# Kernel tuning notes

Hardware: AMD Instinct MI355X
Metric: run time of the kernel (lower is better)

Reference implementation:

```python
import jax, jax.numpy as jnp
import numpy as np

N = 100000      # nodes
IN_DIM = 128    # input feature dim
HID = 64        # hidden_dim / out_dim per head
HEADS = 4
E_RAND = 1600000  # random edges; self-loops appended -> E = E_RAND + N
SCALES = 3


def setup_inputs() -> dict:
    key = jax.random.key(0)
    ks = jax.random.split(key, 12)
    h = jax.random.normal(ks[0], (N, IN_DIM), dtype=jnp.float32)
    src = jax.random.randint(ks[1], (E_RAND,), 0, N)
    dst = jax.random.randint(ks[2], (E_RAND,), 0, N)
    loop = jnp.arange(N)
    src = jnp.concatenate([src, loop])  # self-loops ensure every dst has a mailbox
    dst = jnp.concatenate([dst, loop])
    frac_cover_mat = jax.random.randint(ks[3], (N, SCALES), 0, N)
    # learned params (bias=False everywhere); xavier-ish scaling
    layer1_fc = jax.random.normal(ks[4], (HEADS, HID, IN_DIM), jnp.float32) / np.sqrt(IN_DIM)
    layer1_attn = jax.random.normal(ks[5], (HEADS, 2 * HID), jnp.float32) * 0.1
    layer2_fc = jax.random.normal(ks[6], (HID, HID * HEADS), jnp.float32) / np.sqrt(HID * HEADS)
    layer2_attn = jax.random.normal(ks[7], (2 * HID,), jnp.float32) * 0.1
    frac_w = jax.random.normal(ks[8], (SCALES, HID, IN_DIM), jnp.float32) / np.sqrt(IN_DIM)
    frac_final_w = jax.random.normal(ks[9], (HID, SCALES * HID), jnp.float32) / np.sqrt(SCALES * HID)
    fc2_w = jax.random.normal(ks[10], (HID, 2 * HID), jnp.float32) / np.sqrt(2 * HID)
    return {"h": h, "src": src, "dst": dst, "frac_cover_mat": frac_cover_mat,
            "layer1_fc": layer1_fc, "layer1_attn": layer1_attn,
            "layer2_fc": layer2_fc, "layer2_attn": layer2_attn,
            "frac_w": frac_w, "frac_final_w": frac_final_w, "fc2_w": fc2_w}


def _gat_layer(z, src, dst, attn_w, n):
    # attn(cat([z_src, z_dst])) == z_src @ a_src + z_dst @ a_dst  (bias-free Linear)
    d = z.shape[1]
    e = jax.nn.leaky_relu(z[src] @ attn_w[:d] + z[dst] @ attn_w[d:])  # [E]
    # segment softmax over incoming edges of each dst node
    m = jax.ops.segment_max(e, dst, num_segments=n)
    ex = jnp.exp(e - m[dst])
    denom = jax.ops.segment_sum(ex, dst, num_segments=n)
    alpha = ex / denom[dst]                                   # [E]
    return jax.ops.segment_sum(alpha[:, None] * z[src], dst, num_segments=n)  # [N, d]


def reference(h, src, dst, frac_cover_mat,
              layer1_fc, layer1_attn, layer2_fc, layer2_attn,
              frac_w, frac_final_w, fc2_w):
    n = h.shape[0]
    # layer1: multi-head GAT, merge='cat'
    heads = []
    for i in range(layer1_fc.shape[0]):
        z = h @ layer1_fc[i].T                                # [N, HID]
        heads.append(_gat_layer(z, src, dst, layer1_attn[i], n))
    h_nei = jax.nn.elu(jnp.concatenate(heads, axis=1))        # [N, HID*HEADS]
    # layer2: single-head GAT
    z2 = h_nei @ layer2_fc.T                                  # [N, HID]
    h_nei = _gat_layer(z2, src, dst, layer2_attn, n)          # [N, HID]
    # fractal layer (dropout = identity in eval)
    h_all = [h[frac_cover_mat[:, s]] @ frac_w[s].T for s in range(frac_w.shape[0])]
    h_frac = jnp.concatenate(h_all, axis=1) @ frac_final_w.T  # [N, HID]
    # fc2 on cat([h_nei, h_frac]); dropout identity
    h_global = jnp.concatenate([h_nei, h_frac], axis=1) @ fc2_w.T  # [N, HID]
    # AvgPooling over single graph -> [1, HID]
    return jnp.mean(h_global, axis=0, keepdims=True)
```

## Files before the change

kernel.cpp:

```cpp
#include <hip/hip_runtime.h>
#include <math.h>


#define CAP 128

typedef unsigned int  uint_t;
typedef unsigned short ushort_t;
typedef __attribute__((ext_vector_type(8))) short short8;
typedef __attribute__((ext_vector_type(4))) float floatx4;
typedef __attribute__((ext_vector_type(2))) float floatx2;

__device__ __forceinline__ unsigned xcc_id(){
  unsigned x;
  asm volatile("s_getreg_b32 %0, hwreg(HW_REG_XCC_ID)" : "=s"(x));
  return x & 7u;
}
__device__ __forceinline__ float wred_sum(float v){
#pragma unroll
  for (int o = 1; o < 64; o <<= 1) v += __shfl_xor(v, o, 64);
  return v;
}
__device__ __forceinline__ float lrelu(float x){ return x >= 0.f ? x : 0.01f*x; }
__device__ __forceinline__ ushort_t f2b(float f){
  uint_t u = __float_as_uint(f);
  u = (u + 0x7FFFu + ((u >> 16) & 1u)) >> 16;
  return (ushort_t)u;
}
__device__ __forceinline__ float b2f_lo(uint_t w){ return __uint_as_float(w << 16); }
__device__ __forceinline__ float b2f_hi(uint_t w){ return __uint_as_float(w & 0xFFFF0000u); }

__device__ __forceinline__ void agg8(uint2 u, float4 al,
    floatx2& c00, floatx2& c01, floatx2& c10, floatx2& c11){
  floatx2 p0 = __builtin_amdgcn_cvt_pk_f32_fp8(u.x, false);
  floatx2 p1 = __builtin_amdgcn_cvt_pk_f32_fp8(u.x, true);
  floatx2 p2 = __builtin_amdgcn_cvt_pk_f32_fp8(u.y, false);
  floatx2 p3 = __builtin_amdgcn_cvt_pk_f32_fp8(u.y, true);
  floatx2 aXY = {al.x, al.y}, aZW = {al.z, al.w};
  c00 += aXY * p0;
  c01 += aZW * p1;
  c10 += aXY * p2;
  c11 += aZW * p3;
}

__global__ void k_prep(const float* __restrict__ W1, const float* __restrict__ W2,
                       const float* __restrict__ a1, const float* __restrict__ a2,
                       const int* __restrict__ dstI, int E,
                       const int* __restrict__ fcm, int N3, int* __restrict__ cnt,
                       ushort_t* __restrict__ w1bp, float* __restrict__ v2,
                       int* __restrict__ deg8, int* __restrict__ rk, int PAD){
  __shared__ float v[8][128];
  const int bx = blockIdx.x, t = threadIdx.x;
  if (bx < 128){
    int idx = bx*256 + t;
    int j = idx & 7, lane = (idx >> 3) & 63, ks = (idx >> 9) & 3, tt = idx >> 11;
    int n = tt*16 + (lane & 15), k = ks*32 + (lane >> 4)*8 + j;
    int hh = tt >> 2, m = tt & 3;
    int pt = (m < 2) ? (hh*2 + m) : (8 + hh*2 + (m - 2));
    w1bp[((pt*4 + ks)*64 + lane)*8 + j] = f2b(W1[n*128 + k]);
  } else if (bx == 128){
    for (int o = t; o < 1024; o += 256){
      int col = o >> 7, k = o & 127, hh = col & 3, off = (col >> 2)*64;
      float s = 0.f;
      for (int n = 0; n < 64; n++) s += a1[hh*128 + off + n] * W1[(hh*64 + n)*128 + k];
      v[col][k] = s;
    }
    __syncthreads();
    for (int idx = t; idx < 2048; idx += 256){
      int j = idx & 7, lane = (idx >> 3) & 63, ks = idx >> 9;
      int col = lane & 15, k = ks*32 + (lane >> 4)*8 + j;
      w1bp[32768 + idx] = (col < 8) ? f2b(v[col][k]) : (ushort_t)0;
    }
  } else if (bx == 129){
    float s0 = 0.f, s1 = 0.f;
    for (int j = 0; j < 64; j++){
      float wjk = W2[j*256 + t];
      s0 += wjk * a2[j];
      s1 += wjk * a2[64 + j];
    }
    v2[t] = s0; v2[256 + t] = s1;
  } else {
    const int nb = gridDim.x - 130;
    const unsigned xcd = xcc_id();
    int* myDeg = deg8 + (size_t)xcd * PAD;
    for (int i = (bx-130)*256 + t; i < E; i += nb*256){
      int d = dstI[i];
      int r = __hip_atomic_fetch_add(&myDeg[d], 1, __ATOMIC_RELAXED,
                                     __HIP_MEMORY_SCOPE_WORKGROUP);
      rk[i] = (int)((xcd << 28) | (unsigned)r);
    }
    for (int i = (bx-130)*256 + t; i < N3; i += nb*256){
      int v3 = fcm[i];
      atomicAdd(&cnt[v3*3 + (i % 3)], 1);
    }
  }
}

__global__ __launch_bounds__(256) void k_scan1(const int* __restrict__ deg8,
    int* __restrict__ part, int PAD){
  __shared__ int tmp[256];
  int t = threadIdx.x, i = blockIdx.x*256 + t;
  int v = 0;
#pragma unroll
  for (int x = 0; x < 8; x++) v += deg8[(size_t)x*PAD + i];
  tmp[t] = v;
  __syncthreads();
  for (int off = 128; off > 0; off >>= 1){
    if (t < off) tmp[t] += tmp[t+off];
    __syncthreads();
  }
  if (t == 0) part[blockIdx.x] = tmp[0];
}
__global__ __launch_bounds__(512) void k_scan2(int* __restrict__ part, int B){
  __shared__ int tmp[512];
  int t = threadIdx.x;
  int v = (t < B) ? part[t] : 0;
  tmp[t] = v; __syncthreads();
  for (int off = 1; off < 512; off <<= 1){
    int x = (t >= off) ? tmp[t-off] : 0;
    __syncthreads();
    tmp[t] += x;
    __syncthreads();
  }
  if (t < B) part[t] = tmp[t] - v;
}
__global__ __launch_bounds__(256) void k_scan3(const int* __restrict__ deg8,
    const int* __restrict__ part, int* __restrict__ rowptr,
    int* __restrict__ base8, int PAD){
  __shared__ int tmp[256];
  int t = threadIdx.x, i = blockIdx.x*256 + t;
  int d8[8]; int v = 0;
#pragma unroll
  for (int x = 0; x < 8; x++){ d8[x] = deg8[(size_t)x*PAD + i]; v += d8[x]; }
  tmp[t] = v; __syncthreads();
  for (int off = 1; off < 256; off <<= 1){
    int x = (t >= off) ? tmp[t-off] : 0;
    __syncthreads();
    tmp[t] += x;
    __syncthreads();
  }
  int excl = tmp[t] - v + part[blockIdx.x];
  rowptr[i] = excl;
  int run = excl;
#pragma unroll
  for (int x = 0; x < 8; x++){ base8[(size_t)x*PAD + i] = run; run += d8[x]; }
}

__global__ __launch_bounds__(512, 4) void k_mega(const float* __restrict__ h,
    const ushort_t* __restrict__ w1bp,
    uint_t* __restrict__ z8, float* __restrict__ s1s, float* __restrict__ s1d, int N,
    const int* __restrict__ srcI, const int* __restrict__ dstI,
    const int* __restrict__ rk, const int* __restrict__ base8, int PAD,
    int* __restrict__ csr, int E,
    int Gg, int Gs, int G, int step,
    const int* __restrict__ cnt, float* __restrict__ accFrac)
{
  static __shared__ __align__(16) char smem[36864];
  const int tid = threadIdx.x;
  const int id = (int)(((unsigned long long)blockIdx.x * (unsigned)step) % (unsigned)G);
  if (id < Gg){
    ushort_t* ldsB = (ushort_t*)smem;
    const int wave = tid >> 6, lane = tid & 63;
    const int quad = lane >> 4, l16 = lane & 15;
    const int row0 = id*128 + wave*16;
    const bool act = row0 < N;
    const int ar = act ? ((row0 + l16 < N) ? (row0 + l16) : (N - 1)) : 0;
    short8 AHI[4], ALO[4];
    if (act){
#pragma unroll
      for (int ks = 0; ks < 4; ks++){
        const float* ap = &h[(size_t)ar*128 + ks*32 + quad*8];
        float4 v0 = *(const float4*)ap;
        float4 v1 = *(const float4*)(ap + 4);
        float vv[8] = {v0.x,v0.y,v0.z,v0.w,v1.x,v1.y,v1.z,v1.w};
#pragma unroll
        for (int j = 0; j < 8; j++){
          ushort_t hb = f2b(vv[j]);
          float hf = __uint_as_float((uint_t)hb << 16);
          AHI[ks][j] = (short)hb;
          ALO[ks][j] = (short)f2b(vv[j] - hf);
        }
      }
    }
#pragma unroll
    for (int half = 0; half < 2; half++){
      __syncthreads();
      {
        const int cnt4 = half ? 2304 : 2048;
        const uint4* src = (const uint4*)w1bp + (half ? 2048 : 0);
        uint4* dst = (uint4*)ldsB;
        for (int i = tid; i < cnt4; i += 512) dst[i] = src[i];
      }
      __syncthreads();
      if (!act) continue;
      const int nt = half ? 9 : 8;
      floatx4 c[9];
#pragma unroll
      for (int i = 0; i < 9; i++) c[i] = (floatx4){0.f,0.f,0.f,0.f};
#pragma unroll
      for (int ks = 0; ks < 4; ks++){
        for (int i = 0; i < nt; i++){
          short8 b = *(const short8*)&ldsB[(size_t)((i*4 + ks)*64 + lane)*8];
          c[i] = __builtin_amdgcn_mfma_f32_16x16x32_bf16(AHI[ks], b, c[i], 0, 0, 0);
        }
        if (half){
          short8 b = *(const short8*)&ldsB[(size_t)((8*4 + ks)*64 + lane)*8];
          c[8] = __builtin_amdgcn_mfma_f32_16x16x32_bf16(ALO[ks], b, c[8], 0, 0, 0);
        }
      }
      const int m0 = half ? 2 : 0;
#pragma unroll
      for (int i = 0; i < 4; i++){
        const int r = row0 + quad*4 + i;
        if (r >= N) continue;
#pragma unroll
        for (int dm = 0; dm < 2; dm++){
          int u = 0;
          u = __builtin_amdgcn_cvt_pk_fp8_f32(c[0*2+dm][i], c[1*2+dm][i], u, false);
          u = __builtin_amdgcn_cvt_pk_fp8_f32(c[2*2+dm][i], c[3*2+dm][i], u, true);
          z8[(size_t)r*64 + (m0+dm)*16 + l16] = (uint_t)u;
        }
        if (half){
          const float sv = c[8][i];
          if (l16 < 4) s1s[r*4 + l16] = sv;
          else if (l16 < 8) s1d[r*4 + (l16 - 4)] = sv;
        }
      }
    }
  } else if (id < Gg + Gs){
    const int i = (id - Gg)*512 + tid;
    if (i < E){
      const int d = dstI[i];
      const uint_t u = (uint_t)rk[i];
      const int p = base8[(size_t)(u >> 28)*PAD + d] + (int)(u & 0x0FFFFFFFu);
      csr[p] = srcI[i];
    }
  } else {
    float (*red)[384] = (float(*)[384])smem;
    const int wave = tid >> 6, lane = tid & 63;
    const int g = lane >> 5, li = lane & 31;
    const int Gf = G - Gg - Gs;
    const int stream0 = (id - Gg - Gs)*16 + wave*2 + g;
    const int step16 = Gf * 16;
    float4 a0 = {0,0,0,0}, a1 = {0,0,0,0}, a2 = {0,0,0,0};
    for (int n = stream0; n < N; n += step16){
      const float w0 = (float)cnt[n*3];
      const float w1 = (float)cnt[n*3+1];
      const float w2 = (float)cnt[n*3+2];
      float4 v = *(const float4*)&h[(size_t)n*128 + li*4];
      a0.x += w0*v.x; a0.y += w0*v.y; a0.z += w0*v.z; a0.w += w0*v.w;
      a1.x += w1*v.x; a1.y += w1*v.y; a1.z += w1*v.z; a1.w += w1*v.w;
      a2.x += w2*v.x; a2.y += w2*v.y; a2.z += w2*v.z; a2.w += w2*v.w;
    }
    const int w16 = wave*2 + g;
    *(float4*)&red[w16][0*128 + li*4] = a0;
    *(float4*)&red[w16][1*128 + li*4] = a1;
    *(float4*)&red[w16][2*128 + li*4] = a2;
    __syncthreads();
    for (int i = tid; i < 384; i += 512){
      float v = 0.f;
#pragma unroll
      for (int w = 0; w < 16; w++) v += red[w][i];
      atomicAdd(&accFrac[i], v);
    }
  }
}

__global__ __launch_bounds__(256) void k_gat1(
    const uint_t* __restrict__ z8, const float* __restrict__ s1src, const float* __restrict__ s1dst,
    const int* __restrict__ rowptr, const int* __restrict__ csr, const float* __restrict__ v2,
    uint_t* __restrict__ hneib, float* __restrict__ s2s, float* __restrict__ s2d, int N, int dbase)
{
  __shared__ int   sbuf[4][CAP];
  __shared__ __align__(16) float4 ebuf[4][CAP];
  __shared__ float v2s[512];
  const int tid = threadIdx.x;
  v2s[tid] = v2[tid];
  v2s[tid + 256] = v2[tid + 256];
  __syncthreads();
  const int wave = tid >> 6, lane = tid & 63;
  const int dst = (dbase + blockIdx.x)*4 + wave;
  if (dst >= N) return;
  const int beg = rowptr[dst];
  const int deg = rowptr[dst+1] - beg;
  const float4 sd = *(const float4*)&s1dst[dst*4];
  float t0=0.f,t1=0.f,t2=0.f,t3=0.f;
  for (int j = lane; j < deg; j += 64){
    int s = csr[beg+j];
    float4 sv = *(const float4*)&s1src[s*4];
    float4 a;
    a.x = __expf(lrelu(sv.x+sd.x)); a.y = __expf(lrelu(sv.y+sd.y));
    a.z = __expf(lrelu(sv.z+sd.z)); a.w = __expf(lrelu(sv.w+sd.w));
    if (j < CAP){ sbuf[wave][j] = s*64; ebuf[wave][j] = a; }
    t0 += a.x; t1 += a.y; t2 += a.z; t3 += a.w;
  }
  const float inv[4] = {1.f/wred_sum(t0), 1.f/wred_sum(t1), 1.f/wred_sum(t2), 1.f/wred_sum(t3)};
  const int eh = lane >> 5, li = lane & 31;
  floatx2 c00 = {0.f,0.f}, c01 = {0.f,0.f}, c10 = {0.f,0.f}, c11 = {0.f,0.f};
  if (deg <= CAP){
    const int j0 = (eh < deg) ? eh : 0;
    int offc = sbuf[wave][j0];
    float4 alc = ebuf[wave][j0];
    uint2 uc = *((const uint2*)(z8 + offc) + li);
    for (int jj = 0; jj + 2 <= deg; jj += 2){
      const int jn = jj + 2 + eh;
      const int jnc = (jn < deg) ? jn : (jj + eh);
      const int offn = sbuf[wave][jnc];
      const float4 aln = ebuf[wave][jnc];
      const uint2 un = *((const uint2*)(z8 + offn) + li);
      agg8(uc, alc, c00, c01, c10, c11);
      uc = un; alc = aln;
    }
    if ((deg & 1) && eh == 0)
      agg8(uc, alc, c00, c01, c10, c11);
  } else {
    for (int jj = 0; jj < deg; jj += 2){
      const int j = jj + eh;
      const bool v = j < deg;
      const int jc = v ? j : jj;
      int off; float4 al;
      if (jc < CAP){ off = sbuf[wave][jc]; al = ebuf[wave][jc]; }
      else {
        int s = csr[beg+jc];
        off = s*64;
        float4 sv = *(const float4*)&s1src[s*4];
        al.x = __expf(lrelu(sv.x+sd.x)); al.y = __expf(lrelu(sv.y+sd.y));
        al.z = __expf(lrelu(sv.z+sd.z)); al.w = __expf(lrelu(sv.w+sd.w));
      }
      if (!v){ al.x=0.f; al.y=0.f; al.z=0.f; al.w=0.f; }
      uint2 u = *((const uint2*)(z8 + off) + li);
      agg8(u, al, c00, c01, c10, c11);
    }
  }
  float acc[2][4] = {{c00.x, c00.y, c01.x, c01.y},
                     {c10.x, c10.y, c11.x, c11.y}};
#pragma unroll
  for (int k = 0; k < 2; k++)
#pragma unroll
    for (int hh = 0; hh < 4; hh++) acc[k][hh] += __shfl_xor(acc[k][hh], 32, 64);
  const float* vv = &v2s[eh*256];
  float p = 0.f;
#pragma unroll
  for (int hh = 0; hh < 4; hh++){
    float e0 = acc[0][hh]*inv[hh]; e0 = e0 > 0.f ? e0 : expm1f(e0);
    float e1 = acc[1][hh]*inv[hh]; e1 = e1 > 0.f ? e1 : expm1f(e1);
    p += e0 * vv[hh*64 + 2*li] + e1 * vv[hh*64 + 2*li + 1];
    if ((hh >> 1) == eh)
      hneib[(size_t)dst*128 + hh*32 + li] = (uint_t)f2b(e0) | ((uint_t)f2b(e1) << 16);
  }
#pragma unroll
  for (int o = 1; o < 32; o <<= 1) p += __shfl_xor(p, o, 64);
  if (lane == 0)  s2s[dst] = p;
  if (lane == 32) s2d[dst] = p;
}

__global__ __launch_bounds__(256) void k_aw2(
    const float* __restrict__ s2s, const float* __restrict__ s2d,
    const int* __restrict__ rowptr, const int* __restrict__ csr,
    float* __restrict__ wsrc8, int N)
{
  __shared__ int   sbuf[4][CAP];
  __shared__ float ebuf[4][CAP];
  const unsigned xcd = xcc_id();
  float* ws = wsrc8 + (size_t)xcd * N;
  const int wave = threadIdx.x >> 6, lane = threadIdx.x & 63;
  const int dst = blockIdx.x*4 + wave;
  if (dst >= N) return;
  const int beg = rowptr[dst], deg = rowptr[dst+1] - beg;
  const float sd = s2d[dst];
  float ts = 0.f;
  for (int j = lane; j < deg; j += 64){
    int s = csr[beg+j];
    float a = __expf(lrelu(s2s[s] + sd));
    if (j < CAP){ sbuf[wave][j] = s; ebuf[wave][j] = a; }
    ts += a;
  }
  const float inv = 1.f/wred_sum(ts);
  for (int j = lane; j < deg; j += 64){
    int s; float a;
    if (j < CAP){ s = sbuf[wave][j]; a = ebuf[wave][j]; }
    else { s = csr[beg+j]; a = __expf(lrelu(s2s[s] + sd)); }
    __hip_atomic_fetch_add(&ws[s], a * inv, __ATOMIC_RELAXED,
                           __HIP_MEMORY_SCOPE_WORKGROUP);
  }
}

__global__ __launch_bounds__(256) void k_hsum(const uint_t* __restrict__ hneib,
    const float* __restrict__ wsrc8, float* __restrict__ acc256, int N)
{
  __shared__ float pr[512];
  const int t = threadIdx.x;
  const int h2 = t >> 7, p = t & 127;
  float a0 = 0.f, a1 = 0.f;
  const int step = gridDim.x * 2;
  for (int n = blockIdx.x*2 + h2; n < N; n += step){
    float wn = 0.f;
#pragma unroll
    for (int x = 0; x < 8; x++) wn += wsrc8[(size_t)x*N + n];
    uint_t u = hneib[(size_t)n*128 + p];
    a0 += wn * b2f_lo(u);
    a1 += wn * b2f_hi(u);
  }
  pr[h2*256 + 2*p]     = a0;
  pr[h2*256 + 2*p + 1] = a1;
  __syncthreads();
  float v = pr[t] + pr[256 + t];
  int pp = t >> 1;
  int d = (pp >> 5)*64 + 2*(pp & 31) + (t & 1);
  atomicAdd(&acc256[d], v);
}

__global__ __launch_bounds__(256) void k_finalize(const float* __restrict__ acc256,
    const float* __restrict__ accFrac, const float* __restrict__ W2,
    const float* __restrict__ frw, const float* __restrict__ frf,
    const float* __restrict__ fc2, float* __restrict__ out, float invN)
{
  __shared__ float mh[256], nei[64], g[384], mm[192], hfrac[64];
  int t = threadIdx.x;
  mh[t] = acc256[t] * invN;
  for (int i = t; i < 384; i += 256) g[i] = accFrac[i] * invN;
  __syncthreads();
  if (t < 64){
    float s = 0.f;
    for (int k = 0; k < 256; k++) s += W2[t*256 + k] * mh[k];
    nei[t] = s;
  }
  for (int i = t; i < 192; i += 256){
    int s = i >> 6, d = i & 63;
    const float* w = frw + (size_t)(s*64 + d)*128;
    const float* gs = g + s*128;
    float sum = 0.f;
    for (int k = 0; k < 128; k++) sum += gs[k]*w[k];
    mm[i] = sum;
  }
  __syncthreads();
  if (t < 64){
    float s = 0.f;
    for (int k = 0; k < 192; k++) s += mm[k]*frf[t*192 + k];
    hfrac[t] = s;
  }
  __syncthreads();
  if (t < 64){
    float o = 0.f;
    for (int k = 0; k < 64; k++)
      o += fc2[t*128 + k]*nei[k] + fc2[t*128 + 64 + k]*hfrac[k];
    out[t] = o;
  }
}

extern "C" void kernel_launch(void* const* d_in, const int* in_sizes, int n_in,
                              void* d_out, int out_size, void* d_ws, size_t ws_size,
                              hipStream_t stream)
{
  const float* h    = (const float*)d_in[0];
  const int*   srcI = (const int*)  d_in[1];
  const int*   dstI = (const int*)  d_in[2];
  const int*   fcm  = (const int*)  d_in[3];
  const float* l1fc = (const float*)d_in[4];
  const float* l1at = (const float*)d_in[5];
  const float* l2fc = (const float*)d_in[6];
  const float* l2at = (const float*)d_in[7];
  const float* frw  = (const float*)d_in[8];
  const float* frf  = (const float*)d_in[9];
  const float* fc2  = (const float*)d_in[10];
  float* out = (float*)d_out;
  (void)n_in; (void)out_size; (void)ws_size;

  const int N = in_sizes[0] / 128;
  const int E = in_sizes[1];
  const int B = (N + 256) / 256;
  const int PAD = B * 256;

  char* w = (char*)d_ws;
  size_t off = 0;
  auto alloc = [&](size_t bytes) -> char* {
    char* p = w + off; off = (off + bytes + 255) & ~(size_t)255; return p;
  };
  uint_t* z8    = (uint_t*)alloc((size_t)N*64*4);
  uint_t* hneib = (uint_t*)alloc((size_t)N*128*4);
  int*    rk    = (int*)hneib;
  float* s1s  = (float*)alloc((size_t)N*4*4);
  float* s1d  = (float*)alloc((size_t)N*4*4);
  float* s2s  = (float*)alloc((size_t)N*4);
  float* s2d  = (float*)alloc((size_t)N*4);
  int*   deg8    = (int*)  alloc((size_t)8*PAD*4);
  int*   cnt     = (int*)  alloc((size_t)N*3*4);
  float* wsrc8   = (float*)alloc((size_t)8*N*4);
  float* acc256  = (float*)alloc(256*4);
  float* accFrac = (float*)alloc(384*4);
  const size_t zbytes = (size_t)((char*)accFrac + 384*4 - (char*)deg8);
  int*   rowptr = (int*)alloc((size_t)PAD*4);
  int*   base8  = (int*)alloc((size_t)8*PAD*4);
  int*   part   = (int*)alloc(512*4);
  int*   csr    = (int*)alloc((size_t)E*4);
  ushort_t* w1bp = (ushort_t*)alloc(34816*2);
  float* v2     = (float*)alloc(512*4);

  hipMemsetAsync(deg8, 0, zbytes, stream);

  hipLaunchKernelGGL(k_prep,  dim3(130 + 512), dim3(256), 0, stream,
                     l1fc, l2fc, l1at, l2at, dstI, E, fcm, 3*N, cnt, w1bp, v2,
                     deg8, rk, PAD);
  hipLaunchKernelGGL(k_scan1, dim3(B),   dim3(256), 0, stream, deg8, part, PAD);
  hipLaunchKernelGGL(k_scan2, dim3(1),   dim3(512), 0, stream, part, B);
  hipLaunchKernelGGL(k_scan3, dim3(B),   dim3(256), 0, stream, deg8, part,
                     rowptr, base8, PAD);

  const int Gg = (N + 127) / 128;
  const int Gs = (E + 511) / 512;
  const int Gf = 512;
  const int G  = Gg + Gs + Gf;
  int step = (int)(G * 0.618) | 1;
  auto gcd = [](int a, int b){ while (b){ int t = a % b; a = b; b = t; } return a; };
  while (gcd(step, G) != 1) step += 2;

  hipLaunchKernelGGL(k_mega,  dim3(G), dim3(512), 0, stream,
                     h, w1bp, z8, s1s, s1d, N,
                     srcI, dstI, rk, base8, PAD, csr, E, Gg, Gs, G, step,
                     cnt, accFrac);
  const int nb  = (N + 3) / 4;
  const int nb3 = nb / 3;
  hipLaunchKernelGGL(k_gat1,  dim3(nb3),        dim3(256), 0, stream,
                     z8, s1s, s1d, rowptr, csr, v2, hneib, s2s, s2d, N, 0);
  hipLaunchKernelGGL(k_gat1,  dim3(nb3),        dim3(256), 0, stream,
                     z8, s1s, s1d, rowptr, csr, v2, hneib, s2s, s2d, N, nb3);
  hipLaunchKernelGGL(k_gat1,  dim3(nb - 2*nb3), dim3(256), 0, stream,
                     z8, s1s, s1d, rowptr, csr, v2, hneib, s2s, s2d, N, 2*nb3);
  hipLaunchKernelGGL(k_aw2,   dim3(nb),         dim3(256), 0, stream,
                     s2s, s2d, rowptr, csr, wsrc8, N);
  hipLaunchKernelGGL(k_hsum,  dim3(608),        dim3(256), 0, stream,
                     hneib, wsrc8, acc256, N);
  hipLaunchKernelGGL(k_finalize, dim3(1),       dim3(256), 0, stream,
                     acc256, accFrac, l2fc, frw, frf, fc2, out, 1.0f/(float)N);
}
```

Baseline: 527.4 us.

## Replace layer-2 float scatter atomics with a source-sorted CSC gather sum

Layer-2 per-source weights used to be accumulated with float atomics into per-XCD copies of a weight array. They are now built from a second, source-keyed CSC: k_mega gains a block group that counts source degrees and ranks, and scan kernels build source row pointers. k_aw2 writes each normalized alpha into its CSC slot, and a new k_wsum kernel sums each source's slots. This removes contended float atomics and the 8-way partial reduction, at the cost of extra index arrays, more memory traffic, three more scan launches and one more kernel. The k_gat1 split also changes from three launches to two.

```diff
diff --git a/kernel.cpp b/kernel.cpp
--- a/kernel.cpp
+++ b/kernel.cpp
@@ -95,13 +95,13 @@
   }
 }
 
-__global__ __launch_bounds__(256) void k_scan1(const int* __restrict__ deg8,
+__global__ __launch_bounds__(256) void k_scan1(const int* __restrict__ dp,
     int* __restrict__ part, int PAD){
   __shared__ int tmp[256];
   int t = threadIdx.x, i = blockIdx.x*256 + t;
   int v = 0;
 #pragma unroll
-  for (int x = 0; x < 8; x++) v += deg8[(size_t)x*PAD + i];
+  for (int x = 0; x < 8; x++) v += dp[(size_t)x*PAD + i];
   tmp[t] = v;
   __syncthreads();
   for (int off = 128; off > 0; off >>= 1){
@@ -123,14 +123,14 @@
   }
   if (t < B) part[t] = tmp[t] - v;
 }
-__global__ __launch_bounds__(256) void k_scan3(const int* __restrict__ deg8,
-    const int* __restrict__ part, int* __restrict__ rowptr,
-    int* __restrict__ base8, int PAD){
+__global__ __launch_bounds__(256) void k_scan3(const int* __restrict__ dp,
+    const int* __restrict__ part, int* __restrict__ rowp,
+    int* __restrict__ basep, int PAD){
   __shared__ int tmp[256];
   int t = threadIdx.x, i = blockIdx.x*256 + t;
   int d8[8]; int v = 0;
 #pragma unroll
-  for (int x = 0; x < 8; x++){ d8[x] = deg8[(size_t)x*PAD + i]; v += d8[x]; }
+  for (int x = 0; x < 8; x++){ d8[x] = dp[(size_t)x*PAD + i]; v += d8[x]; }
   tmp[t] = v; __syncthreads();
   for (int off = 1; off < 256; off <<= 1){
     int x = (t >= off) ? tmp[t-off] : 0;
@@ -139,10 +139,10 @@
     __syncthreads();
   }
   int excl = tmp[t] - v + part[blockIdx.x];
-  rowptr[i] = excl;
+  rowp[i] = excl;
   int run = excl;
 #pragma unroll
-  for (int x = 0; x < 8; x++){ base8[(size_t)x*PAD + i] = run; run += d8[x]; }
+  for (int x = 0; x < 8; x++){ basep[(size_t)x*PAD + i] = run; run += d8[x]; }
 }
 
 __global__ __launch_bounds__(512, 4) void k_mega(const float* __restrict__ h,
@@ -150,8 +150,9 @@
     uint_t* __restrict__ z8, float* __restrict__ s1s, float* __restrict__ s1d, int N,
     const int* __restrict__ srcI, const int* __restrict__ dstI,
     const int* __restrict__ rk, const int* __restrict__ base8, int PAD,
-    int* __restrict__ csr, int E,
-    int Gg, int Gs, int G, int step,
+    int* __restrict__ csr, int* __restrict__ csrEid,
+    int* __restrict__ degS8, int* __restrict__ rkS, int E,
+    int Gg, int Gs, int Gh, int G, int step,
     const int* __restrict__ cnt, float* __restrict__ accFrac)
 {
   static __shared__ __align__(16) char smem[36864];
@@ -231,15 +232,25 @@
     if (i < E){
       const int d = dstI[i];
       const uint_t u = (uint_t)rk[i];
-      const int p = base8[(size_t)(u >> 28)*PAD + d] + (int)(u & 0x0FFFFFFFu);
-      csr[p] = srcI[i];
+      const int pD = base8[(size_t)(u >> 28)*PAD + d] + (int)(u & 0x0FFFFFFFu);
+      csr[pD]    = srcI[i];
+      csrEid[pD] = i;
+    }
+  } else if (id < Gg + Gs + Gh){
+    const int i = (id - Gg - Gs)*512 + tid;
+    if (i < E){
+      const unsigned xcd = xcc_id();
+      int s = srcI[i];
+      int rs = __hip_atomic_fetch_add(&degS8[(size_t)xcd*PAD + s], 1,
+                                      __ATOMIC_RELAXED, __HIP_MEMORY_SCOPE_WORKGROUP);
+      rkS[i] = (int)((xcd << 28) | (unsigned)rs);
     }
   } else {
     float (*red)[384] = (float(*)[384])smem;
     const int wave = tid >> 6, lane = tid & 63;
     const int g = lane >> 5, li = lane & 31;
-    const int Gf = G - Gg - Gs;
-    const int stream0 = (id - Gg - Gs)*16 + wave*2 + g;
+    const int Gf = G - Gg - Gs - Gh;
+    const int stream0 = (id - Gg - Gs - Gh)*16 + wave*2 + g;
     const int step16 = Gf * 16;
     float4 a0 = {0,0,0,0}, a1 = {0,0,0,0}, a2 = {0,0,0,0};
     for (int n = stream0; n < N; n += step16){
@@ -356,12 +367,12 @@
 __global__ __launch_bounds__(256) void k_aw2(
     const float* __restrict__ s2s, const float* __restrict__ s2d,
     const int* __restrict__ rowptr, const int* __restrict__ csr,
-    float* __restrict__ wsrc8, int N)
+    const int* __restrict__ csrEid, const int* __restrict__ rkS,
+    const int* __restrict__ baseS8, int PAD,
+    float* __restrict__ alphaCSC, int N)
 {
   __shared__ int   sbuf[4][CAP];
   __shared__ float ebuf[4][CAP];
-  const unsigned xcd = xcc_id();
-  float* ws = wsrc8 + (size_t)xcd * N;
   const int wave = threadIdx.x >> 6, lane = threadIdx.x & 63;
   const int dst = blockIdx.x*4 + wave;
   if (dst >= N) return;
@@ -379,13 +390,26 @@
     int s; float a;
     if (j < CAP){ s = sbuf[wave][j]; a = ebuf[wave][j]; }
     else { s = csr[beg+j]; a = __expf(lrelu(s2s[s] + sd)); }
-    __hip_atomic_fetch_add(&ws[s], a * inv, __ATOMIC_RELAXED,
-                           __HIP_MEMORY_SCOPE_WORKGROUP);
-  }
+    const int eid = csrEid[beg+j];
+    const uint_t u = (uint_t)rkS[eid];
+    const int pS = baseS8[(size_t)(u >> 28)*PAD + s] + (int)(u & 0x0FFFFFFFu);
+    alphaCSC[pS] = a * inv;
+  }
+}
+
+__global__ __launch_bounds__(256) void k_wsum(const float* __restrict__ alphaCSC,
+    const int* __restrict__ rowptrS, float* __restrict__ wsrc, int N)
+{
+  const int n = blockIdx.x*256 + threadIdx.x;
+  if (n >= N) return;
+  const int b = rowptrS[n], e = rowptrS[n+1];
+  float s = 0.f;
+  for (int k = b; k < e; k++) s += alphaCSC[k];
+  wsrc[n] = s;
 }
 
 __global__ __launch_bounds__(256) void k_hsum(const uint_t* __restrict__ hneib,
-    const float* __restrict__ wsrc8, float* __restrict__ acc256, int N)
+    const float* __restrict__ wsrc, float* __restrict__ acc256, int N)
 {
   __shared__ float pr[512];
   const int t = threadIdx.x;
@@ -393,9 +417,7 @@
   float a0 = 0.f, a1 = 0.f;
   const int step = gridDim.x * 2;
   for (int n = blockIdx.x*2 + h2; n < N; n += step){
-    float wn = 0.f;
-#pragma unroll
-    for (int x = 0; x < 8; x++) wn += wsrc8[(size_t)x*N + n];
+    float wn = wsrc[n];
     uint_t u = hneib[(size_t)n*128 + p];
     a0 += wn * b2f_lo(u);
     a1 += wn * b2f_hi(u);
@@ -483,15 +505,22 @@
   float* s2s  = (float*)alloc((size_t)N*4);
   float* s2d  = (float*)alloc((size_t)N*4);
   int*   deg8    = (int*)  alloc((size_t)8*PAD*4);
+  int*   degS8   = (int*)  alloc((size_t)8*PAD*4);
   int*   cnt     = (int*)  alloc((size_t)N*3*4);
-  float* wsrc8   = (float*)alloc((size_t)8*N*4);
   float* acc256  = (float*)alloc(256*4);
   float* accFrac = (float*)alloc(384*4);
   const size_t zbytes = (size_t)((char*)accFrac + 384*4 - (char*)deg8);
-  int*   rowptr = (int*)alloc((size_t)PAD*4);
-  int*   base8  = (int*)alloc((size_t)8*PAD*4);
-  int*   part   = (int*)alloc(512*4);
-  int*   csr    = (int*)alloc((size_t)E*4);
+  int*   rowptr  = (int*)alloc((size_t)PAD*4);
+  int*   rowptrS = (int*)alloc((size_t)PAD*4);
+  int*   base8   = (int*)alloc((size_t)8*PAD*4);
+  int*   baseS8  = (int*)alloc((size_t)8*PAD*4);
+  int*   partD   = (int*)alloc(512*4);
+  int*   partS   = (int*)alloc(512*4);
+  int*   csr     = (int*)alloc((size_t)E*4);
+  int*   csrEid  = (int*)alloc((size_t)E*4);
+  int*   rkS     = (int*)alloc((size_t)E*4);
+  float* alphaCSC= (float*)alloc((size_t)E*4);
+  float* wsrc    = (float*)alloc((size_t)N*4);
   ushort_t* w1bp = (ushort_t*)alloc(34816*2);
   float* v2     = (float*)alloc(512*4);
 
@@ -500,35 +529,41 @@
   hipLaunchKernelGGL(k_prep,  dim3(130 + 512), dim3(256), 0, stream,
                      l1fc, l2fc, l1at, l2at, dstI, E, fcm, 3*N, cnt, w1bp, v2,
                      deg8, rk, PAD);
-  hipLaunchKernelGGL(k_scan1, dim3(B),   dim3(256), 0, stream, deg8, part, PAD);
-  hipLaunchKernelGGL(k_scan2, dim3(1),   dim3(512), 0, stream, part, B);
-  hipLaunchKernelGGL(k_scan3, dim3(B),   dim3(256), 0, stream, deg8, part,
+  hipLaunchKernelGGL(k_scan1, dim3(B), dim3(256), 0, stream, deg8, partD, PAD);
+  hipLaunchKernelGGL(k_scan2, dim3(1), dim3(512), 0, stream, partD, B);
+  hipLaunchKernelGGL(k_scan3, dim3(B), dim3(256), 0, stream, deg8, partD,
                      rowptr, base8, PAD);
 
   const int Gg = (N + 127) / 128;
   const int Gs = (E + 511) / 512;
+  const int Gh = (E + 511) / 512;
   const int Gf = 512;
-  const int G  = Gg + Gs + Gf;
+  const int G  = Gg + Gs + Gh + Gf;
   int step = (int)(G * 0.618) | 1;
   auto gcd = [](int a, int b){ while (b){ int t = a % b; a = b; b = t; } return a; };
   while (gcd(step, G) != 1) step += 2;
 
   hipLaunchKernelGGL(k_mega,  dim3(G), dim3(512), 0, stream,
                      h, w1bp, z8, s1s, s1d, N,
-                     srcI, dstI, rk, base8, PAD, csr, E, Gg, Gs, G, step,
-                     cnt, accFrac);
+                     srcI, dstI, rk, base8, PAD, csr, csrEid, degS8, rkS, E,
+                     Gg, Gs, Gh, G, step, cnt, accFrac);
+  hipLaunchKernelGGL(k_scan1, dim3(B), dim3(256), 0, stream, degS8, partS, PAD);
+  hipLaunchKernelGGL(k_scan2, dim3(1), dim3(512), 0, stream, partS, B);
+  hipLaunchKernelGGL(k_scan3, dim3(B), dim3(256), 0, stream, degS8, partS,
+                     rowptrS, baseS8, PAD);
+
   const int nb  = (N + 3) / 4;
-  const int nb3 = nb / 3;
-  hipLaunchKernelGGL(k_gat1,  dim3(nb3),        dim3(256), 0, stream,
+  const int nb1 = nb / 2;
+  hipLaunchKernelGGL(k_gat1,  dim3(nb1),      dim3(256), 0, stream,
                      z8, s1s, s1d, rowptr, csr, v2, hneib, s2s, s2d, N, 0);
-  hipLaunchKernelGGL(k_gat1,  dim3(nb3),        dim3(256), 0, stream,
-                     z8, s1s, s1d, rowptr, csr, v2, hneib, s2s, s2d, N, nb3);
-  hipLaunchKernelGGL(k_gat1,  dim3(nb - 2*nb3), dim3(256), 0, stream,
-                     z8, s1s, s1d, rowptr, csr, v2, hneib, s2s, s2d, N, 2*nb3);
-  hipLaunchKernelGGL(k_aw2,   dim3(nb),         dim3(256), 0, stream,
-                     s2s, s2d, rowptr, csr, wsrc8, N);
-  hipLaunchKernelGGL(k_hsum,  dim3(608),        dim3(256), 0, stream,
-                     hneib, wsrc8, acc256, N);
-  hipLaunchKernelGGL(k_finalize, dim3(1),       dim3(256), 0, stream,
+  hipLaunchKernelGGL(k_gat1,  dim3(nb - nb1), dim3(256), 0, stream,
+                     z8, s1s, s1d, rowptr, csr, v2, hneib, s2s, s2d, N, nb1);
+  hipLaunchKernelGGL(k_aw2,   dim3(nb),       dim3(256), 0, stream,
+                     s2s, s2d, rowptr, csr, csrEid, rkS, baseS8, PAD, alphaCSC, N);
+  hipLaunchKernelGGL(k_wsum,  dim3((N+255)/256), dim3(256), 0, stream,
+                     alphaCSC, rowptrS, wsrc, N);
+  hipLaunchKernelGGL(k_hsum,  dim3(608),      dim3(256), 0, stream,
+                     hneib, wsrc, acc256, N);
+  hipLaunchKernelGGL(k_finalize, dim3(1),     dim3(256), 0, stream,
                      acc256, accFrac, l2fc, frw, frf, fc2, out, 1.0f/(float)N);
 }
```

Result: slower. 562.3 us (+6.6%).
